# Kernel optimization log

Hardware: AMD Instinct MI355X
Metric: run time of the kernel (lower is better)

Reference implementation:

```python
import jax, jax.numpy as jnp
import numpy as np

# Assumptions (SubNetwork / SelfAttention source not provided):
#  - SubNetwork(in_dim, hidden, 3) is a VectorNet polyline subgraph: 3 layers of
#    (Linear->ReLU) followed by maxpool-over-nodes concat, so per-node dim -> 2*hidden.
#    Layer in-dims: in_dim, 2h, 2h; the graph argument is structural and unused in the math.
#  - SelfAttention(D, D) is single-head scaled dot-product self-attention returning
#    (output, attn_weights); the [0] in forward selects the output.
#  - map_mask is all ones, so max_mask == M and every map polyline is processed.

def _nan0(x):
    return jnp.where(jnp.isnan(x), jnp.zeros_like(x), x)

def _subnet(x, Ws, Bs):
    # x: [G, T, N, in] -> per-graph global feature [G, T, 2h]
    for W, b in zip(Ws, Bs):
        h = jax.nn.relu(x @ W + b)                       # [G,T,N,h]
        agg = jnp.max(h, axis=2, keepdims=True)           # [G,T,1,h]
        x = jnp.concatenate([h, jnp.broadcast_to(agg, h.shape)], axis=-1)
    return jnp.max(x, axis=2)                             # [G,T,2h]


def setup_inputs() -> dict:
    key = jax.random.key(0)
    ks = jax.random.split(key, 32)
    in_dim, h, D, out_dim = 16, 64, 128, 60
    A, M, O, T, Na, Nm, No = 4, 64, 32, 32, 256, 256, 128

    def w(k, shape, fan_in):
        return jax.random.normal(k, shape, dtype=jnp.float32) / np.sqrt(fan_in).astype(np.float32)

    inp = {
        'agent_set': jnp.zeros((A, 1), jnp.float32),
        'map_set': jnp.zeros((M, 1), jnp.float32),
        'agent_feature': jax.random.normal(ks[0], (A, T, Na, in_dim), dtype=jnp.float32),
        'map_feature': jax.random.normal(ks[1], (M, T, Nm, in_dim), dtype=jnp.float32),
        'map_mask': jnp.ones((T, M), jnp.int32),
        'obj_set': jnp.zeros((O, 1), jnp.float32),
        'obj_feature': jax.random.normal(ks[2], (O, T, No, in_dim), dtype=jnp.float32),
    }
    # subnetwork params (agent / map / obj)
    names = ['a', 'm', 'o']
    for i, n in enumerate(names):
        base = 3 + i * 3
        inp[n + 'W0'] = w(ks[base + 0], (in_dim, h), in_dim)
        inp[n + 'B0'] = jnp.zeros((h,), jnp.float32)
        inp[n + 'W1'] = w(ks[base + 1], (2 * h, h), 2 * h)
        inp[n + 'B1'] = jnp.zeros((h,), jnp.float32)
        inp[n + 'W2'] = w(ks[base + 2], (2 * h, h), 2 * h)
        inp[n + 'B2'] = jnp.zeros((h,), jnp.float32)
    inp['Wq'] = w(ks[12], (D, D), D)
    inp['Wk'] = w(ks[13], (D, D), D)
    inp['Wv'] = w(ks[14], (D, D), D)
    inp['mlpW1'] = w(ks[15], (A, D, D), D)
    inp['mlpB1'] = jnp.zeros((A, D), jnp.float32)
    inp['mlpW2'] = w(ks[16], (A, D, out_dim), D)
    inp['mlpB2'] = jnp.zeros((A, out_dim), jnp.float32)
    return inp


def reference(agent_set, map_set, agent_feature, map_feature, map_mask, obj_set, obj_feature,
              aW0, aB0, aW1, aB1, aW2, aB2,
              mW0, mB0, mW1, mB1, mW2, mB2,
              oW0, oB0, oW1, oB1, oW2, oB2,
              Wq, Wk, Wv, mlpW1, mlpB1, mlpW2, mlpB2):
    af = _nan0(agent_feature)
    ag = _subnet(af, (aW0, aW1, aW2), (aB0, aB1, aB2))    # [A,T,D]
    # original only NaN-masks the first agent's global feature
    ag = jnp.concatenate([_nan0(ag[:1]), ag[1:]], axis=0)
    # map_mask rows all sum to M -> max_mask == M, use all map polylines
    mg = _subnet(map_feature, (mW0, mW1, mW2), (mB0, mB1, mB2))  # [M,T,D]
    og = _subnet(obj_feature, (oW0, oW1, oW2), (oB0, oB1, oB2))  # [O,T,D]
    G = jnp.concatenate([ag, mg, og], axis=0)              # [E,T,D]
    x = jnp.transpose(G, (1, 0, 2))                        # [T,E,D]
    q, k, v = x @ Wq, x @ Wk, x @ Wv
    scale = np.float32(1.0 / np.sqrt(x.shape[-1]))
    attn = jax.nn.softmax(jnp.einsum('ted,tfd->tef', q, k) * scale, axis=-1)
    o = jnp.einsum('tef,tfd->ted', attn, v)                # [T,E,D]
    hdn = jnp.tanh(jnp.einsum('ted,adh->ateh', o, mlpW1) + mlpB1[:, None, None, :])
    out = jnp.einsum('ateh,aho->ateo', hdn, mlpW2) + mlpB2[:, None, None, :]
    return out  # [num_agents=4, T, E, out_dim]
```

## Files before the change

### kernel.cpp

```cpp
#include <hip/hip_runtime.h>
#include <hip/hip_fp16.h>

#define TT 32
#define EN 100
#define DD 128

typedef _Float16 half4 __attribute__((ext_vector_type(4)));
typedef _Float16 half2v __attribute__((ext_vector_type(2)));
typedef float f32x4 __attribute__((ext_vector_type(4)));

#define MFMA16(a, b, c) __builtin_amdgcn_mfma_f32_16x16x16f16((a), (b), (c), 0, 0, 0)

__device__ __forceinline__ float nan0f(float v) { return (v == v) ? v : 0.f; }

__device__ __forceinline__ float ftanh(float x) {
    x = fminf(9.f, fmaxf(-9.f, x));
    float e = __expf(2.f * x);
    return (e - 1.f) / (e + 1.f);
}

__device__ __forceinline__ half2v pk2(float lo, float hi) {
    auto v = __builtin_amdgcn_cvt_pkrtz(lo, hi);
    half2v r;
    __builtin_memcpy(&r, &v, 4);
    return r;
}

__device__ __forceinline__ int ldsoff(int ps, int row, int col) {
    int b = (col >> 6) * ps + row * 136 + ((col & 63) << 1);
    return b ^ ((row & 12) << 2);
}

__device__ __forceinline__ int hoff(int row, int col) {
    return (row * 136 + (col << 1)) ^ ((row & 12) << 2);
}

#define OFF_AW   0
#define OFF_MW   2304
#define OFF_OW   4608
#define OFF_QKV  6912
#define OFF_MW1  19200
#define OFF_MW2  35584

struct PackArgs {
    const float* src[20];
    int C[20], VC[20], ktc[20], ntc[20], dsto[20], ar[20];
};

__global__ __launch_bounds__(256) void pack_w(PackArgs pa, _Float16* __restrict__ dst)
{
    const int s = blockIdx.y;
    const int total = pa.ktc[s] * pa.ntc[s] * 64;
    const int i = blockIdx.x * 256 + threadIdx.x;
    if (i >= total) return;
    const int ml = i & 15, gq = (i >> 4) & 3, rest = i >> 6;
    const int ntc = pa.ntc[s];
    const int nt = rest % ntc, kt = rest / ntc;
    const int col = nt * 16 + ml, row0 = kt * 16 + gq * 4;
    const float* W = pa.src[s];
    const int C = pa.C[s], VC = pa.VC[s], ar = pa.ar[s];
    half4 v;
#pragma unroll
    for (int j = 0; j < 4; ++j) {
        float fv = 0.f;
        if (col < VC) {
            fv = W[(size_t)(row0 + j) * C + col];
            if (ar) fv += W[(size_t)(row0 + j + ar) * C + col];
        }
        v[j] = (_Float16)fv;
    }
    *(half4*)(dst + ((size_t)pa.dsto[s] + i) * 4) = v;
}

struct SubArgs {
    const float* feat[3];
    const _Float16* wp[3];
    const float* B0[3];
    const float* W1[3]; const float* B1[3];
    const float* W2[3]; const float* B2[3];
    int e_base[3];
    int lo[3];
    int dn[3];
};

__global__ __launch_bounds__(512, 4) void subnet_uber(SubArgs sa, _Float16* __restrict__ xh)
{
    const int bid = blockIdx.x;
    const int s = (bid >= sa.lo[1]) + (bid >= sa.lo[2]);
    const int tid = threadIdx.x;
    const int w = tid >> 6, lane = tid & 63, ml = lane & 15, gq = lane >> 4;
    const bool hm = (s == 2);
    const int h = hm ? (w >> 2) : 0;
    const int wl = hm ? (w & 3) : w;
    const int idx = hm ? ((bid - sa.lo[2]) * 2 + h) : (bid - sa.lo[s]);
    const int g = idx >> 5, t = idx & 31;
    const int N = hm ? 128 : 256;
    const int rowL = wl * 32;
    const int hsb = h * 128;
    const int grp0 = h * 4;

    __shared__ __attribute__((aligned(16))) unsigned char Hs[256 * 136];
    __shared__ float red[8][64];
    __shared__ float part[8][64];

    f32x4 acc[2][4];
    float cvr[4];

    auto epilogue = [&](bool store) {
#pragma unroll
        for (int nt = 0; nt < 4; ++nt) {
            float am;
            if (store) {
                const half2v zz = {(_Float16)0.f, (_Float16)0.f};
                half2v amh = zz;
#pragma unroll
                for (int mt = 0; mt < 2; ++mt) {
                    f32x4 v = acc[mt][nt];
                    half2v p0 = __builtin_elementwise_max(pk2(v.x, v.y), zz);
                    half2v p1 = __builtin_elementwise_max(pk2(v.z, v.w), zz);
                    amh = __builtin_elementwise_max(
                        amh, __builtin_elementwise_max(p0, p1));
                    const int r0 = hsb + rowL + mt * 16 + gq * 4;
                    const int c = nt * 16 + ml;
                    unsigned u0, u1;
                    __builtin_memcpy(&u0, &p0, 4);
                    __builtin_memcpy(&u1, &p1, 4);
                    *(unsigned short*)(Hs + hoff(r0 + 0, c)) = (unsigned short)u0;
                    *(unsigned short*)(Hs + hoff(r0 + 1, c)) = (unsigned short)(u0 >> 16);
                    *(unsigned short*)(Hs + hoff(r0 + 2, c)) = (unsigned short)u1;
                    *(unsigned short*)(Hs + hoff(r0 + 3, c)) = (unsigned short)(u1 >> 16);
                }
                am = fmaxf((float)amh[0], (float)amh[1]);
            } else {
                am = 0.f;
#pragma unroll
                for (int mt = 0; mt < 2; ++mt) {
                    f32x4 v = acc[mt][nt];
                    am = fmaxf(am, fmaxf(fmaxf(v.x, v.y), fmaxf(v.z, v.w)));
                }
            }
            am = fmaxf(am, __shfl_xor(am, 16, 64));
            am = fmaxf(am, __shfl_xor(am, 32, 64));
            if (lane < 16) red[w][nt * 16 + lane] = am;
        }
        __syncthreads();
    };

    auto group_max = [&]() {
        float a = red[grp0][lane];
#pragma unroll
        for (int ww = 1; ww < 4; ++ww) a = fmaxf(a, red[grp0 + ww][lane]);
        if (!hm) {
#pragma unroll
            for (int ww = 4; ww < 8; ++ww) a = fmaxf(a, red[ww][lane]);
        }
        return a;
    };

    auto make_cvec = [&](const float* Wn, const float* Bn) {
        float a = group_max();
        float sum = 0.f;
        if (hm) {
#pragma unroll
            for (int kk = 0; kk < 16; ++kk) {
                int k = wl * 16 + kk;
                sum = fmaf(__shfl(a, k, 64), Wn[(size_t)(64 + k) * 64 + lane], sum);
            }
        } else {
#pragma unroll
            for (int kk = 0; kk < 8; ++kk) {
                int k = w * 8 + kk;
                sum = fmaf(__shfl(a, k, 64), Wn[(size_t)(64 + k) * 64 + lane], sum);
            }
        }
        part[w][lane] = sum;
        __syncthreads();
        float c = Bn[lane];
#pragma unroll
        for (int ww = 0; ww < 4; ++ww) c += part[grp0 + ww][lane];
        if (!hm) {
#pragma unroll
            for (int ww = 4; ww < 8; ++ww) c += part[ww][lane];
        }
#pragma unroll
        for (int nt = 0; nt < 4; ++nt) cvr[nt] = __shfl(c, nt * 16 + ml, 64);
    };

    const _Float16* wp = sa.wp[s];

    {
        const float* B0 = sa.B0[s];
#pragma unroll
        for (int nt = 0; nt < 4; ++nt) {
            float b = B0[nt * 16 + ml];
            acc[0][nt] = f32x4{b, b, b, b};
            acc[1][nt] = f32x4{b, b, b, b};
        }
        half4 bf[4];
#pragma unroll
        for (int nt = 0; nt < 4; ++nt)
            bf[nt] = *(const half4*)(wp + (size_t)(((nt * 4 + gq) * 16 + ml) * 4));
        const float* xb = sa.feat[s] + (size_t)idx * N * 16;
        const int dn = sa.dn[s];
#pragma unroll
        for (int mt = 0; mt < 2; ++mt) {
            float4 xv = *reinterpret_cast<const float4*>(
                xb + (size_t)(rowL + mt * 16 + ml) * 16 + gq * 4);
            if (dn) {
                xv.x = nan0f(xv.x); xv.y = nan0f(xv.y);
                xv.z = nan0f(xv.z); xv.w = nan0f(xv.w);
            }
            half4 af = half4{(_Float16)xv.x, (_Float16)xv.y,
                             (_Float16)xv.z, (_Float16)xv.w};
#pragma unroll
            for (int nt = 0; nt < 4; ++nt)
                acc[mt][nt] = MFMA16(af, bf[nt], acc[mt][nt]);
        }
    }
    epilogue(true);
    make_cvec(sa.W1[s], sa.B1[s]);

    auto layer = [&](const _Float16* wb, bool store) {
#pragma unroll
        for (int nt = 0; nt < 4; ++nt) {
            float cv = cvr[nt];
            acc[0][nt] = f32x4{cv, cv, cv, cv};
            acc[1][nt] = f32x4{cv, cv, cv, cv};
        }
#pragma unroll
        for (int kt = 0; kt < 4; ++kt) {
            half4 bf[4];
#pragma unroll
            for (int nt = 0; nt < 4; ++nt)
                bf[nt] = *(const half4*)(wb +
                    (size_t)(((((kt * 4 + nt) * 4) + gq) * 16 + ml) * 4));
#pragma unroll
            for (int mt = 0; mt < 2; ++mt) {
                half4 af = *(const half4*)(Hs +
                    hoff(hsb + rowL + mt * 16 + ml, kt * 16 + gq * 4));
#pragma unroll
                for (int nt = 0; nt < 4; ++nt)
                    acc[mt][nt] = MFMA16(af, bf[nt], acc[mt][nt]);
            }
        }
        epilogue(store);
    };

    layer(wp + 256 * 4, true);
    make_cvec(sa.W2[s], sa.B2[s]);
    layer(wp + 1280 * 4, false);

    if (wl == 0) {
        float a = group_max();
        size_t base = ((size_t)t * 112 + (sa.e_base[s] + g)) * 64;
        xh[base + lane] = (_Float16)a;
    }
}

#define PSX 15232
#define WSO 30464

__global__ __launch_bounds__(256) void qkv_kernel(
    const _Float16* __restrict__ xh, const _Float16* __restrict__ wqkv,
    _Float16* __restrict__ qh, _Float16* __restrict__ kh, _Float16* __restrict__ vh)
{
    const int t = blockIdx.x;
    const int tgt = blockIdx.y;
    const int tid = threadIdx.x;
    const int w = tid >> 6, lane = tid & 63, ml = lane & 15, gq = lane >> 4;

    const _Float16* wb = wqkv + (size_t)tgt * 2048 * 4;
    _Float16* Oh = (tgt == 0) ? qh : (tgt == 1) ? kh : vh;

#pragma unroll 1
    for (int mi = 0; mi < 2; ++mi) {
        int mt = w + (mi << 2);
        if (mt >= 7) continue;
        const int srow = min(mt * 16 + ml, EN - 1);
        half4 xa[4];
#pragma unroll
        for (int kt = 0; kt < 4; ++kt)
            xa[kt] = *(const half4*)(xh + (size_t)t * 7168 + srow * 64 + kt * 16 + gq * 4);
#pragma unroll
        for (int nt = 0; nt < 8; ++nt) {
            f32x4 acc = {0.f, 0.f, 0.f, 0.f};
#pragma unroll
            for (int kt = 0; kt < 4; ++kt) {
                half4 b = *(const half4*)(wb +
                    (size_t)(((((kt * 8 + nt) * 4) + gq) * 16 + ml) * 4));
                acc = MFMA16(xa[kt], b, acc);
            }
            _Float16* op = Oh + (size_t)t * 14336 + (mt * 16 + gq * 4) * 128 + nt * 16 + ml;
            op[0]   = (_Float16)acc.x;
            op[128] = (_Float16)acc.y;
            op[256] = (_Float16)acc.z;
            op[384] = (_Float16)acc.w;
        }
    }
}

#define VSO 30464

__global__ __launch_bounds__(256) void attn_kernel(
    const _Float16* __restrict__ qh, const _Float16* __restrict__ kh,
    const _Float16* __restrict__ vh, float* __restrict__ obuf)
{
    const int t = blockIdx.x;
    const int rb = blockIdx.y;
    const int tid = threadIdx.x;
    const int w = tid >> 6, lane = tid & 63, ml = lane & 15, gq = lane >> 4;

    __shared__ __attribute__((aligned(16))) unsigned char sm[2 * WSO];

    for (int i = tid; i < 112 * 32; i += 256) {
        int row = i >> 5, c4 = (i & 31) << 2;
        size_t src = (size_t)t * 14336 + row * 128 + c4;
        *(half4*)(sm + ldsoff(PSX, row, c4))       = *(const half4*)(kh + src);
        *(half4*)(sm + VSO + ldsoff(PSX, row, c4)) = *(const half4*)(vh + src);
    }
    __syncthreads();

    const float scale = 0.088388347648318447f;
    const int mt = rb * 4 + w;
    const bool act = mt < 7;
    half4 pf[7];

    if (act) {
        half4 qa[8];
#pragma unroll
        for (int kt = 0; kt < 8; ++kt)
            qa[kt] = *(const half4*)(qh + (size_t)t * 14336 + (mt * 16 + ml) * 128
                                     + kt * 16 + gq * 4);
        f32x4 sacc[7];
#pragma unroll
        for (int nt = 0; nt < 7; ++nt) {
            f32x4 acc = {0.f, 0.f, 0.f, 0.f};
#pragma unroll
            for (int kt = 0; kt < 8; ++kt) {
                half4 b = *(const half4*)(sm + ldsoff(PSX, nt * 16 + ml, kt * 16 + gq * 4));
                acc = MFMA16(qa[kt], b, acc);
            }
            sacc[nt].x = acc.x * scale; sacc[nt].y = acc.y * scale;
            sacc[nt].z = acc.z * scale; sacc[nt].w = acc.w * scale;
        }
        float mx[4] = {-3e38f, -3e38f, -3e38f, -3e38f};
#pragma unroll
        for (int nt = 0; nt < 7; ++nt) {
            if (nt < 6 || ml < 4) {
                mx[0] = fmaxf(mx[0], sacc[nt].x); mx[1] = fmaxf(mx[1], sacc[nt].y);
                mx[2] = fmaxf(mx[2], sacc[nt].z); mx[3] = fmaxf(mx[3], sacc[nt].w);
            }
        }
#pragma unroll
        for (int m = 1; m <= 8; m <<= 1) {
#pragma unroll
            for (int i = 0; i < 4; ++i) mx[i] = fmaxf(mx[i], __shfl_xor(mx[i], m, 64));
        }
        float sum[4] = {0.f, 0.f, 0.f, 0.f};
#pragma unroll
        for (int nt = 0; nt < 7; ++nt) {
            bool v = (nt < 6) || (ml < 4);
            float p0 = v ? __expf(sacc[nt].x - mx[0]) : 0.f;
            float p1 = v ? __expf(sacc[nt].y - mx[1]) : 0.f;
            float p2 = v ? __expf(sacc[nt].z - mx[2]) : 0.f;
            float p3 = v ? __expf(sacc[nt].w - mx[3]) : 0.f;
            sum[0] += p0; sum[1] += p1; sum[2] += p2; sum[3] += p3;
            sacc[nt] = f32x4{p0, p1, p2, p3};
        }
#pragma unroll
        for (int m = 1; m <= 8; m <<= 1) {
#pragma unroll
            for (int i = 0; i < 4; ++i) sum[i] += __shfl_xor(sum[i], m, 64);
        }
        float inv[4] = {1.f / sum[0], 1.f / sum[1], 1.f / sum[2], 1.f / sum[3]};
#pragma unroll
        for (int nt = 0; nt < 7; ++nt)
            pf[nt] = half4{(_Float16)(sacc[nt].x * inv[0]), (_Float16)(sacc[nt].y * inv[1]),
                           (_Float16)(sacc[nt].z * inv[2]), (_Float16)(sacc[nt].w * inv[3])};
    }

    __syncthreads();

    if (act) {
        const int row0 = mt * 16 + gq * 4;
#pragma unroll
        for (int nt = 0; nt < 7; ++nt) {
            const int col = nt * 16 + ml;
            *(_Float16*)(sm + ldsoff(PSX, row0 + 0, col)) = pf[nt].x;
            *(_Float16*)(sm + ldsoff(PSX, row0 + 1, col)) = pf[nt].y;
            *(_Float16*)(sm + ldsoff(PSX, row0 + 2, col)) = pf[nt].z;
            *(_Float16*)(sm + ldsoff(PSX, row0 + 3, col)) = pf[nt].w;
        }
    }
    __syncthreads();

    if (act) {
        half4 pa[7];
#pragma unroll
        for (int kt = 0; kt < 7; ++kt)
            pa[kt] = *(const half4*)(sm + ldsoff(PSX, mt * 16 + ml, kt * 16 + gq * 4));
#pragma unroll
        for (int nt = 0; nt < 8; ++nt) {
            f32x4 acc = {0.f, 0.f, 0.f, 0.f};
            const int col = nt * 16 + ml;
#pragma unroll
            for (int kt = 0; kt < 7; ++kt) {
                const int r0 = kt * 16 + gq * 4;
                half4 b = half4{
                    *(const _Float16*)(sm + VSO + ldsoff(PSX, r0 + 0, col)),
                    *(const _Float16*)(sm + VSO + ldsoff(PSX, r0 + 1, col)),
                    *(const _Float16*)(sm + VSO + ldsoff(PSX, r0 + 2, col)),
                    *(const _Float16*)(sm + VSO + ldsoff(PSX, r0 + 3, col))};
                acc = MFMA16(pa[kt], b, acc);
            }
            const int row0 = mt * 16 + gq * 4;
            float* op = obuf + (size_t)t * EN * DD + row0 * DD + col;
            if (row0 + 0 < EN) op[0]       = acc.x;
            if (row0 + 1 < EN) op[DD]      = acc.y;
            if (row0 + 2 < EN) op[2 * DD]  = acc.z;
            if (row0 + 3 < EN) op[3 * DD]  = acc.w;
        }
    }
}

#define PSH 8704

__global__ __launch_bounds__(256) void mlp_kernel(
    const float* __restrict__ obuf, const _Float16* __restrict__ wpk,
    const float* __restrict__ B1, const float* __restrict__ B2,
    float* __restrict__ out)
{
    const int a = blockIdx.y;
    const int tid = threadIdx.x;
    const int w = tid >> 6, lane = tid & 63, ml = lane & 15, gq = lane >> 4;
    const int rowbase = blockIdx.x * 64 + w * 16;

    __shared__ __attribute__((aligned(16))) unsigned char sm[PSH * 2];

    const _Float16* w1b = wpk + ((size_t)OFF_MW1 + a * 4096) * 4;
    const _Float16* w2b = wpk + ((size_t)OFF_MW2 + a * 2048) * 4;

    half4 xa[8];
#pragma unroll
    for (int kt = 0; kt < 8; ++kt) {
        float4 f = *reinterpret_cast<const float4*>(
            obuf + (size_t)(rowbase + ml) * 128 + kt * 16 + gq * 4);
        xa[kt] = half4{(_Float16)f.x, (_Float16)f.y, (_Float16)f.z, (_Float16)f.w};
    }
#pragma unroll
    for (int nt = 0; nt < 8; ++nt) {
        const int col = nt * 16 + ml;
        float bv = B1[a * 128 + col];
        f32x4 acc = {bv, bv, bv, bv};
#pragma unroll
        for (int kt = 0; kt < 8; ++kt) {
            half4 b = *(const half4*)(w1b +
                (size_t)(((((kt * 8 + nt) * 4) + gq) * 16 + ml) * 4));
            acc = MFMA16(xa[kt], b, acc);
        }
        const int lr0 = w * 16 + gq * 4;
        *(_Float16*)(sm + ldsoff(PSH, lr0 + 0, col)) = (_Float16)ftanh(acc.x);
        *(_Float16*)(sm + ldsoff(PSH, lr0 + 1, col)) = (_Float16)ftanh(acc.y);
        *(_Float16*)(sm + ldsoff(PSH, lr0 + 2, col)) = (_Float16)ftanh(acc.z);
        *(_Float16*)(sm + ldsoff(PSH, lr0 + 3, col)) = (_Float16)ftanh(acc.w);
    }

    half4 ha[8];
#pragma unroll
    for (int kt = 0; kt < 8; ++kt)
        ha[kt] = *(const half4*)(sm + ldsoff(PSH, w * 16 + ml, kt * 16 + gq * 4));
#pragma unroll
    for (int nt = 0; nt < 4; ++nt) {
        const int o = nt * 16 + ml;
        const bool valid = o < 60;
        float bv = valid ? B2[a * 60 + o] : 0.f;
        f32x4 acc = {bv, bv, bv, bv};
#pragma unroll
        for (int kt = 0; kt < 8; ++kt) {
            half4 b = *(const half4*)(w2b +
                (size_t)(((((kt * 4 + nt) * 4) + gq) * 16 + ml) * 4));
            acc = MFMA16(ha[kt], b, acc);
        }
        if (valid) {
            float* op = out + (size_t)a * 192000 + (size_t)(rowbase + gq * 4) * 60 + o;
            op[0]   = acc.x;
            op[60]  = acc.y;
            op[120] = acc.z;
            op[180] = acc.w;
        }
    }
}

extern "C" void kernel_launch(void* const* d_in, const int* in_sizes, int n_in,
                              void* d_out, int out_size, void* d_ws, size_t ws_size,
                              hipStream_t stream)
{
    const float* agent_feature = (const float*)d_in[2];
    const float* map_feature   = (const float*)d_in[3];
    const float* obj_feature   = (const float*)d_in[6];
    const float* aW0 = (const float*)d_in[7];  const float* aB0 = (const float*)d_in[8];
    const float* aW1 = (const float*)d_in[9];  const float* aB1 = (const float*)d_in[10];
    const float* aW2 = (const float*)d_in[11]; const float* aB2 = (const float*)d_in[12];
    const float* mW0 = (const float*)d_in[13]; const float* mB0 = (const float*)d_in[14];
    const float* mW1 = (const float*)d_in[15]; const float* mB1 = (const float*)d_in[16];
    const float* mW2 = (const float*)d_in[17]; const float* mB2 = (const float*)d_in[18];
    const float* oW0 = (const float*)d_in[19]; const float* oB0 = (const float*)d_in[20];
    const float* oW1 = (const float*)d_in[21]; const float* oB1 = (const float*)d_in[22];
    const float* oW2 = (const float*)d_in[23]; const float* oB2 = (const float*)d_in[24];
    const float* Wq = (const float*)d_in[25];
    const float* Wk = (const float*)d_in[26];
    const float* Wv = (const float*)d_in[27];
    const float* mlpW1 = (const float*)d_in[28]; const float* mlpB1 = (const float*)d_in[29];
    const float* mlpW2 = (const float*)d_in[30]; const float* mlpB2 = (const float*)d_in[31];

    _Float16* xh  = (_Float16*)d_ws;
    _Float16* qh  = xh + 229376;
    _Float16* kh  = qh + 458752;
    _Float16* vh  = kh + 458752;
    float* obuf   = (float*)(vh + 458752);
    _Float16* wpk = (_Float16*)(obuf + 409600);

    float* outp = (float*)d_out;

    PackArgs pa;
    auto seg = [&](int s, const float* src, int C, int VC, int ktc, int ntc,
                   int dsto, int ar = 0) {
        pa.src[s] = src; pa.C[s] = C; pa.VC[s] = VC;
        pa.ktc[s] = ktc; pa.ntc[s] = ntc; pa.dsto[s] = dsto; pa.ar[s] = ar;
    };
    seg(0, aW0, 64, 64, 1, 4, OFF_AW);
    seg(1, aW1, 64, 64, 4, 4, OFF_AW + 256);
    seg(2, aW2, 64, 64, 4, 4, OFF_AW + 1280);
    seg(3, mW0, 64, 64, 1, 4, OFF_MW);
    seg(4, mW1, 64, 64, 4, 4, OFF_MW + 256);
    seg(5, mW2, 64, 64, 4, 4, OFF_MW + 1280);
    seg(6, oW0, 64, 64, 1, 4, OFF_OW);
    seg(7, oW1, 64, 64, 4, 4, OFF_OW + 256);
    seg(8, oW2, 64, 64, 4, 4, OFF_OW + 1280);
    seg(9,  Wq, 128, 128, 4, 8, OFF_QKV,        64);
    seg(10, Wk, 128, 128, 4, 8, OFF_QKV + 2048, 64);
    seg(11, Wv, 128, 128, 4, 8, OFF_QKV + 4096, 64);
    for (int a = 0; a < 4; ++a) {
        seg(12 + a, mlpW1 + (size_t)a * 16384, 128, 128, 8, 8, OFF_MW1 + a * 4096);
        seg(16 + a, mlpW2 + (size_t)a * 7680,  60,  60,  8, 4, OFF_MW2 + a * 2048);
    }
    pack_w<<<dim3(16, 20), 256, 0, stream>>>(pa, wpk);

    SubArgs sa;
    sa.feat[0] = agent_feature; sa.feat[1] = map_feature; sa.feat[2] = obj_feature;
    sa.wp[0] = wpk + OFF_AW * 4; sa.wp[1] = wpk + OFF_MW * 4; sa.wp[2] = wpk + OFF_OW * 4;
    sa.B0[0] = aB0; sa.B0[1] = mB0; sa.B0[2] = oB0;
    sa.W1[0] = aW1; sa.W1[1] = mW1; sa.W1[2] = oW1;
    sa.B1[0] = aB1; sa.B1[1] = mB1; sa.B1[2] = oB1;
    sa.W2[0] = aW2; sa.W2[1] = mW2; sa.W2[2] = oW2;
    sa.B2[0] = aB2; sa.B2[1] = mB2; sa.B2[2] = oB2;
    sa.e_base[0] = 0; sa.e_base[1] = 4; sa.e_base[2] = 68;
    sa.lo[0] = 0; sa.lo[1] = 128; sa.lo[2] = 128 + 2048;
    sa.dn[0] = 1; sa.dn[1] = 0; sa.dn[2] = 0;
    subnet_uber<<<dim3(2688), 512, 0, stream>>>(sa, xh);

    qkv_kernel<<<dim3(TT, 3), 256, 0, stream>>>(xh, wpk + OFF_QKV * 4, qh, kh, vh);
    attn_kernel<<<dim3(TT, 2), 256, 0, stream>>>(qh, kh, vh, obuf);
    mlp_kernel<<<dim3(50, 4), 256, 0, stream>>>(obuf, wpk, mlpB1, mlpB2, outp);
}
```

Measured before the change: 84.96 us.

## Fuse QKV projection into attention kernel and store attention output as fp16

The separate QKV projection kernel is removed. Each attention block now computes K and V for all rows, plus Q for its own row tile, directly into shared memory, so the q/k/v global round trip and one kernel launch go away. The attention output buffer becomes fp16, which halves the traffic into the MLP kernel and drops its conversion step. In exchange, each of the two row-blocks per timestep recomputes the full K and V projection, and the larger shared-memory footprint may lower occupancy.

```diff
diff --git a/kernel.cpp b/kernel.cpp
--- a/kernel.cpp
+++ b/kernel.cpp
@@ -258,65 +258,56 @@
 }
 
 #define PSX 15232
-#define WSO 30464
-
-__global__ __launch_bounds__(256) void qkv_kernel(
+#define KPO 0
+#define VVO 30464
+#define QSO 60928
+#define PSQ 8704
+
+__global__ __launch_bounds__(256) void attn_fused(
     const _Float16* __restrict__ xh, const _Float16* __restrict__ wqkv,
-    _Float16* __restrict__ qh, _Float16* __restrict__ kh, _Float16* __restrict__ vh)
-{
-    const int t = blockIdx.x;
-    const int tgt = blockIdx.y;
-    const int tid = threadIdx.x;
-    const int w = tid >> 6, lane = tid & 63, ml = lane & 15, gq = lane >> 4;
-
-    const _Float16* wb = wqkv + (size_t)tgt * 2048 * 4;
-    _Float16* Oh = (tgt == 0) ? qh : (tgt == 1) ? kh : vh;
-
-#pragma unroll 1
-    for (int mi = 0; mi < 2; ++mi) {
-        int mt = w + (mi << 2);
-        if (mt >= 7) continue;
-        const int srow = min(mt * 16 + ml, EN - 1);
-        half4 xa[4];
-#pragma unroll
-        for (int kt = 0; kt < 4; ++kt)
-            xa[kt] = *(const half4*)(xh + (size_t)t * 7168 + srow * 64 + kt * 16 + gq * 4);
-#pragma unroll
-        for (int nt = 0; nt < 8; ++nt) {
-            f32x4 acc = {0.f, 0.f, 0.f, 0.f};
-#pragma unroll
-            for (int kt = 0; kt < 4; ++kt) {
-                half4 b = *(const half4*)(wb +
-                    (size_t)(((((kt * 8 + nt) * 4) + gq) * 16 + ml) * 4));
-                acc = MFMA16(xa[kt], b, acc);
-            }
-            _Float16* op = Oh + (size_t)t * 14336 + (mt * 16 + gq * 4) * 128 + nt * 16 + ml;
-            op[0]   = (_Float16)acc.x;
-            op[128] = (_Float16)acc.y;
-            op[256] = (_Float16)acc.z;
-            op[384] = (_Float16)acc.w;
-        }
-    }
-}
-
-#define VSO 30464
-
-__global__ __launch_bounds__(256) void attn_kernel(
-    const _Float16* __restrict__ qh, const _Float16* __restrict__ kh,
-    const _Float16* __restrict__ vh, float* __restrict__ obuf)
+    _Float16* __restrict__ obufh)
 {
     const int t = blockIdx.x;
     const int rb = blockIdx.y;
     const int tid = threadIdx.x;
     const int w = tid >> 6, lane = tid & 63, ml = lane & 15, gq = lane >> 4;
 
-    __shared__ __attribute__((aligned(16))) unsigned char sm[2 * WSO];
-
-    for (int i = tid; i < 112 * 32; i += 256) {
-        int row = i >> 5, c4 = (i & 31) << 2;
-        size_t src = (size_t)t * 14336 + row * 128 + c4;
-        *(half4*)(sm + ldsoff(PSX, row, c4))       = *(const half4*)(kh + src);
-        *(half4*)(sm + VSO + ldsoff(PSX, row, c4)) = *(const half4*)(vh + src);
+    __shared__ __attribute__((aligned(16))) unsigned char sm[78336];
+
+    {
+        half4 xa[4];
+        auto do_tile = [&](int tgt, int dstOff, int ps, int rowb) {
+            const _Float16* wb = wqkv + (size_t)tgt * 2048 * 4;
+#pragma unroll
+            for (int nt = 0; nt < 8; ++nt) {
+                f32x4 acc = {0.f, 0.f, 0.f, 0.f};
+#pragma unroll
+                for (int kt = 0; kt < 4; ++kt) {
+                    half4 b = *(const half4*)(wb +
+                        (size_t)(((((kt * 8 + nt) * 4) + gq) * 16 + ml) * 4));
+                    acc = MFMA16(xa[kt], b, acc);
+                }
+                const int r0 = rowb + gq * 4;
+                const int col = nt * 16 + ml;
+                *(_Float16*)(sm + dstOff + ldsoff(ps, r0 + 0, col)) = (_Float16)acc.x;
+                *(_Float16*)(sm + dstOff + ldsoff(ps, r0 + 1, col)) = (_Float16)acc.y;
+                *(_Float16*)(sm + dstOff + ldsoff(ps, r0 + 2, col)) = (_Float16)acc.z;
+                *(_Float16*)(sm + dstOff + ldsoff(ps, r0 + 3, col)) = (_Float16)acc.w;
+            }
+        };
+#pragma unroll 1
+        for (int mi = 0; mi < 2; ++mi) {
+            const int mt = w + (mi << 2);
+            if (mt >= 7) continue;
+            const int srow = min(mt * 16 + ml, EN - 1);
+#pragma unroll
+            for (int kt = 0; kt < 4; ++kt)
+                xa[kt] = *(const half4*)(xh + (size_t)t * 7168 + srow * 64
+                                         + kt * 16 + gq * 4);
+            do_tile(1, KPO, PSX, mt * 16);
+            do_tile(2, VVO, PSX, mt * 16);
+            if (mi == rb) do_tile(0, QSO, PSQ, w * 16);
+        }
     }
     __syncthreads();
 
@@ -329,15 +320,16 @@
         half4 qa[8];
 #pragma unroll
         for (int kt = 0; kt < 8; ++kt)
-            qa[kt] = *(const half4*)(qh + (size_t)t * 14336 + (mt * 16 + ml) * 128
-                                     + kt * 16 + gq * 4);
+            qa[kt] = *(const half4*)(sm + QSO +
+                ldsoff(PSQ, w * 16 + ml, kt * 16 + gq * 4));
         f32x4 sacc[7];
 #pragma unroll
         for (int nt = 0; nt < 7; ++nt) {
             f32x4 acc = {0.f, 0.f, 0.f, 0.f};
 #pragma unroll
             for (int kt = 0; kt < 8; ++kt) {
-                half4 b = *(const half4*)(sm + ldsoff(PSX, nt * 16 + ml, kt * 16 + gq * 4));
+                half4 b = *(const half4*)(sm + KPO +
+                    ldsoff(PSX, nt * 16 + ml, kt * 16 + gq * 4));
                 acc = MFMA16(qa[kt], b, acc);
             }
             sacc[nt].x = acc.x * scale; sacc[nt].y = acc.y * scale;
@@ -386,10 +378,10 @@
 #pragma unroll
         for (int nt = 0; nt < 7; ++nt) {
             const int col = nt * 16 + ml;
-            *(_Float16*)(sm + ldsoff(PSX, row0 + 0, col)) = pf[nt].x;
-            *(_Float16*)(sm + ldsoff(PSX, row0 + 1, col)) = pf[nt].y;
-            *(_Float16*)(sm + ldsoff(PSX, row0 + 2, col)) = pf[nt].z;
-            *(_Float16*)(sm + ldsoff(PSX, row0 + 3, col)) = pf[nt].w;
+            *(_Float16*)(sm + KPO + ldsoff(PSX, row0 + 0, col)) = pf[nt].x;
+            *(_Float16*)(sm + KPO + ldsoff(PSX, row0 + 1, col)) = pf[nt].y;
+            *(_Float16*)(sm + KPO + ldsoff(PSX, row0 + 2, col)) = pf[nt].z;
+            *(_Float16*)(sm + KPO + ldsoff(PSX, row0 + 3, col)) = pf[nt].w;
         }
     }
     __syncthreads();
@@ -398,7 +390,8 @@
         half4 pa[7];
 #pragma unroll
         for (int kt = 0; kt < 7; ++kt)
-            pa[kt] = *(const half4*)(sm + ldsoff(PSX, mt * 16 + ml, kt * 16 + gq * 4));
+            pa[kt] = *(const half4*)(sm + KPO +
+                ldsoff(PSX, mt * 16 + ml, kt * 16 + gq * 4));
 #pragma unroll
         for (int nt = 0; nt < 8; ++nt) {
             f32x4 acc = {0.f, 0.f, 0.f, 0.f};
@@ -407,18 +400,18 @@
             for (int kt = 0; kt < 7; ++kt) {
                 const int r0 = kt * 16 + gq * 4;
                 half4 b = half4{
-                    *(const _Float16*)(sm + VSO + ldsoff(PSX, r0 + 0, col)),
-                    *(const _Float16*)(sm + VSO + ldsoff(PSX, r0 + 1, col)),
-                    *(const _Float16*)(sm + VSO + ldsoff(PSX, r0 + 2, col)),
-                    *(const _Float16*)(sm + VSO + ldsoff(PSX, r0 + 3, col))};
+                    *(const _Float16*)(sm + VVO + ldsoff(PSX, r0 + 0, col)),
+                    *(const _Float16*)(sm + VVO + ldsoff(PSX, r0 + 1, col)),
+                    *(const _Float16*)(sm + VVO + ldsoff(PSX, r0 + 2, col)),
+                    *(const _Float16*)(sm + VVO + ldsoff(PSX, r0 + 3, col))};
                 acc = MFMA16(pa[kt], b, acc);
             }
             const int row0 = mt * 16 + gq * 4;
-            float* op = obuf + (size_t)t * EN * DD + row0 * DD + col;
-            if (row0 + 0 < EN) op[0]       = acc.x;
-            if (row0 + 1 < EN) op[DD]      = acc.y;
-            if (row0 + 2 < EN) op[2 * DD]  = acc.z;
-            if (row0 + 3 < EN) op[3 * DD]  = acc.w;
+            _Float16* op = obufh + (size_t)t * EN * DD + row0 * DD + col;
+            if (row0 + 0 < EN) op[0]       = (_Float16)acc.x;
+            if (row0 + 1 < EN) op[DD]      = (_Float16)acc.y;
+            if (row0 + 2 < EN) op[2 * DD]  = (_Float16)acc.z;
+            if (row0 + 3 < EN) op[3 * DD]  = (_Float16)acc.w;
         }
     }
 }
@@ -426,7 +419,7 @@
 #define PSH 8704
 
 __global__ __launch_bounds__(256) void mlp_kernel(
-    const float* __restrict__ obuf, const _Float16* __restrict__ wpk,
+    const _Float16* __restrict__ obufh, const _Float16* __restrict__ wpk,
     const float* __restrict__ B1, const float* __restrict__ B2,
     float* __restrict__ out)
 {
@@ -442,11 +435,9 @@
 
     half4 xa[8];
 #pragma unroll
-    for (int kt = 0; kt < 8; ++kt) {
-        float4 f = *reinterpret_cast<const float4*>(
-            obuf + (size_t)(rowbase + ml) * 128 + kt * 16 + gq * 4);
-        xa[kt] = half4{(_Float16)f.x, (_Float16)f.y, (_Float16)f.z, (_Float16)f.w};
-    }
+    for (int kt = 0; kt < 8; ++kt)
+        xa[kt] = *(const half4*)(obufh + (size_t)(rowbase + ml) * 128
+                                 + kt * 16 + gq * 4);
 #pragma unroll
     for (int nt = 0; nt < 8; ++nt) {
         const int col = nt * 16 + ml;
@@ -513,12 +504,9 @@
     const float* mlpW1 = (const float*)d_in[28]; const float* mlpB1 = (const float*)d_in[29];
     const float* mlpW2 = (const float*)d_in[30]; const float* mlpB2 = (const float*)d_in[31];
 
-    _Float16* xh  = (_Float16*)d_ws;
-    _Float16* qh  = xh + 229376;
-    _Float16* kh  = qh + 458752;
-    _Float16* vh  = kh + 458752;
-    float* obuf   = (float*)(vh + 458752);
-    _Float16* wpk = (_Float16*)(obuf + 409600);
+    _Float16* xh    = (_Float16*)d_ws;
+    _Float16* obufh = xh + 229376;
+    _Float16* wpk   = obufh + 409600;
 
     float* outp = (float*)d_out;
 
@@ -559,7 +547,6 @@
     sa.dn[0] = 1; sa.dn[1] = 0; sa.dn[2] = 0;
     subnet_uber<<<dim3(2688), 512, 0, stream>>>(sa, xh);
 
-    qkv_kernel<<<dim3(TT, 3), 256, 0, stream>>>(xh, wpk + OFF_QKV * 4, qh, kh, vh);
-    attn_kernel<<<dim3(TT, 2), 256, 0, stream>>>(qh, kh, vh, obuf);
-    mlp_kernel<<<dim3(50, 4), 256, 0, stream>>>(obuf, wpk, mlpB1, mlpB2, outp);
-}
+    attn_fused<<<dim3(TT, 2), 256, 0, stream>>>(xh, wpk + OFF_QKV * 4, obufh);
+    mlp_kernel<<<dim3(50, 4), 256, 0, stream>>>(obufh, wpk, mlpB1, mlpB2, outp);
+}
```

Result: slower. 104.4 us (median of 2 runs) (+22.9%).
